# Optimization experiments

Hardware: AMD Instinct MI355X
Metric: run time of the kernel (lower is better)

Reference implementation:

```python
import jax, jax.numpy as jnp
import numpy as np

DIM = 2048
DIM_INNER = 4096
D_STATE = 64
D_CONV = 4
HEADDIM = 128
NHEADS = DIM_INNER // HEADDIM  # 32
CHUNK = 256
BATCH = 1
SEQ = 2048
CONV_DIM = DIM_INNER + 2 * D_STATE           # 4224
D_IN_PROJ = 2 * DIM_INNER + 2 * D_STATE + NHEADS  # 8352


def setup_inputs() -> dict:
    key = jax.random.key(0)
    ks = jax.random.split(key, 8)
    x = jax.random.normal(ks[0], (BATCH, SEQ, DIM), jnp.float32)
    in_proj_w = jax.random.normal(ks[1], (D_IN_PROJ, DIM), jnp.float32) * 0.02
    conv_w = jax.random.normal(ks[2], (CONV_DIM, D_CONV), jnp.float32) * 0.2
    conv_b = jnp.zeros((CONV_DIM,), jnp.float32)
    dt_bias = jax.random.normal(ks[3], (NHEADS,), jnp.float32) * 0.1
    A_log = jnp.log(jax.random.uniform(ks[4], (NHEADS,), jnp.float32, 1.0, 16.0))
    D = jnp.ones((NHEADS,), jnp.float32)
    norm_w = jnp.ones((DIM_INNER,), jnp.float32)
    out_proj_w = jax.random.normal(ks[5], (DIM, DIM_INNER), jnp.float32) * 0.02
    return dict(x=x, in_proj_w=in_proj_w, conv_w=conv_w, conv_b=conv_b,
                dt_bias=dt_bias, A_log=A_log, D=D, norm_w=norm_w,
                out_proj_w=out_proj_w)


def _segsum(a):
    # a: [..., T]; out[..., i, j] = sum_{k=j+1..i} a[..., k] for i>=j else -inf
    T = a.shape[-1]
    cs = jnp.cumsum(a, axis=-1)
    seg = cs[..., :, None] - cs[..., None, :]
    mask = jnp.tril(jnp.ones((T, T), bool))
    return jnp.where(mask, seg, -jnp.inf)


def _ssd(x, A, Bm, Cm, chunk):
    # x: [b,l,h,p], A: [b,l,h], Bm/Cm: [b,l,n] (ngroups=1, group dim squeezed)
    b, l, h, p = x.shape
    n = Bm.shape[-1]
    c = l // chunk
    x = x.reshape(b, c, chunk, h, p)
    A = A.reshape(b, c, chunk, h).transpose(0, 3, 1, 2)  # [b,h,c,l]
    Bm = Bm.reshape(b, c, chunk, n)
    Cm = Cm.reshape(b, c, chunk, n)
    A_cumsum = jnp.cumsum(A, axis=-1)                    # [b,h,c,l]
    Lmat = jnp.exp(_segsum(A))                           # [b,h,c,l,l]
    # intra-chunk (diagonal) contribution
    Y_diag = jnp.einsum('bcln,bcsn,bhcls,bcshp->bclhp', Cm, Bm, Lmat, x)
    # per-chunk states
    decay_states = jnp.exp(A_cumsum[..., -1:] - A_cumsum)
    states = jnp.einsum('bcln,bhcl,bclhp->bchpn', Bm, decay_states, x)
    states = jnp.concatenate([jnp.zeros_like(states[:, :1]), states], axis=1)
    # inter-chunk recurrence
    A_last = jnp.pad(A_cumsum[..., -1], ((0, 0), (0, 0), (1, 0)))  # [b,h,c+1]
    decay_chunk = jnp.exp(_segsum(A_last))
    new_states = jnp.einsum('bhzc,bchpn->bzhpn', decay_chunk, states)
    states, final_state = new_states[:, :-1], new_states[:, -1]
    # state -> output (off-diagonal) contribution
    state_decay_out = jnp.exp(A_cumsum)
    Y_off = jnp.einsum('bcln,bchpn,bhcl->bclhp', Cm, states, state_decay_out)
    return (Y_diag + Y_off).reshape(b, l, h, p), final_state


def reference(x, in_proj_w, conv_w, conv_b, dt_bias, A_log, D, norm_w, out_proj_w):
    B, L, _ = x.shape
    zxbcdt = x @ in_proj_w.T                              # [B,L,8352]
    z = zxbcdt[..., :DIM_INNER]
    xBC = zxbcdt[..., DIM_INNER:DIM_INNER + CONV_DIM]
    dt = jax.nn.softplus(zxbcdt[..., -NHEADS:] + dt_bias)  # [B,L,H]
    # causal depthwise conv1d over time (pad d_conv-1 on the left)
    xc = xBC.transpose(0, 2, 1)                           # [B,conv_dim,L]
    xc = jax.lax.conv_general_dilated(
        xc, conv_w[:, None, :], (1,), [(D_CONV - 1, 0)],
        dimension_numbers=('NCH', 'OIH', 'NCH'), feature_group_count=CONV_DIM)
    xc = xc + conv_b[None, :, None]
    xBC = jax.nn.silu(xc).transpose(0, 2, 1)              # [B,L,conv_dim]
    xs = xBC[..., :DIM_INNER].reshape(B, L, NHEADS, HEADDIM)
    Bmat = xBC[..., DIM_INNER:DIM_INNER + D_STATE]
    Cmat = xBC[..., DIM_INNER + D_STATE:]
    A = -jnp.exp(A_log)                                   # [H]
    y, final_state = _ssd(xs * dt[..., None], A * dt, Bmat, Cmat, CHUNK)
    y = y + xs * D[:, None]
    y = y.reshape(B, L, DIM_INNER)
    # gated RMSNorm: x * silu(z), then rms_norm with weight
    g = y * jax.nn.silu(z)
    g = g * jax.lax.rsqrt(jnp.mean(g * g, axis=-1, keepdims=True) + 1e-5) * norm_w
    return g @ out_proj_w.T
```

## Files before the change

### kernel.cpp

```cpp
#include <hip/hip_runtime.h>

typedef short v8s __attribute__((ext_vector_type(8)));
typedef float v4f __attribute__((ext_vector_type(4)));

#define L_SEQ  2048
#define DPROJ  8352
#define CONVD  4224
#define DIN    4096
#define NH     32
#define HD     128
#define NSTATE 64
#define NCHUNK 8
#define CKLEN  256

#define GLOAD_LDS16(gp, lp) \
  __builtin_amdgcn_global_load_lds((const __attribute__((address_space(1))) void*)(gp), \
                                   (__attribute__((address_space(3))) void*)(lp), 16, 0, 0)

__device__ __forceinline__ unsigned short to_bf16(float f) {
  unsigned u = __float_as_uint(f);
  return (unsigned short)((u + 0x7fffu + ((u >> 16) & 1u)) >> 16);
}

__global__ void cvt_bf16_kernel(const float* __restrict__ in,
                                unsigned short* __restrict__ out, int n) {
  int i = (blockIdx.x * 256 + threadIdx.x) * 8;
  if (i + 8 <= n) {
    float4 a = *(const float4*)(in + i);
    float4 b = *(const float4*)(in + i + 4);
    v8s r;
    r[0] = (short)to_bf16(a.x); r[1] = (short)to_bf16(a.y);
    r[2] = (short)to_bf16(a.z); r[3] = (short)to_bf16(a.w);
    r[4] = (short)to_bf16(b.x); r[5] = (short)to_bf16(b.y);
    r[6] = (short)to_bf16(b.z); r[7] = (short)to_bf16(b.w);
    *(v8s*)(out + i) = r;
  }
}


#define BAR    __builtin_amdgcn_s_barrier()
#define SCHEDB __builtin_amdgcn_sched_barrier(0)
#define LGKM0  asm volatile("s_waitcnt lgkmcnt(0)" ::: "memory")
#define VMCNT4 asm volatile("s_waitcnt vmcnt(4)" ::: "memory")

#define RDA(bu, mh) do { \
  _Pragma("unroll") \
  for (int i = 0; i < 4; ++i) \
    _Pragma("unroll") \
    for (int s = 0; s < 2; ++s) { \
      int row_ = (mh) * 128 + wm * 64 + i * 16 + lrow; \
      int off_ = row_ * 128 + s * 64 + lquad * 16; \
      off_ ^= ((off_ >> 9) & 1) << 5; \
      a8[i][s] = *(const v8s*)((const char*)smem + (bu) * 32768 + off_); \
    } \
} while (0)

#define RDB(bu, nh) do { \
  _Pragma("unroll") \
  for (int j = 0; j < 2; ++j) \
    _Pragma("unroll") \
    for (int s = 0; s < 2; ++s) { \
      int row_ = (nh) * 128 + wn * 32 + j * 16 + lrow; \
      int off_ = row_ * 128 + s * 64 + lquad * 16; \
      off_ ^= ((off_ >> 9) & 1) << 5; \
      b8[nh][j][s] = *(const v8s*)((const char*)smem + 65536 + (bu) * 32768 + off_); \
    } \
} while (0)

#define MM(mh, nh) do { \
  __builtin_amdgcn_s_setprio(1); \
  _Pragma("unroll") \
  for (int i = 0; i < 4; ++i) \
    _Pragma("unroll") \
    for (int j = 0; j < 2; ++j) \
      _Pragma("unroll") \
      for (int s = 0; s < 2; ++s) \
        acc[(mh)*4+i][(nh)*2+j] = __builtin_amdgcn_mfma_f32_16x16x32_bf16( \
            a8[i][s], b8[(nh)][j][s], acc[(mh)*4+i][(nh)*2+j], 0, 0, 0); \
  __builtin_amdgcn_s_setprio(0); \
} while (0)

#define KSTEP(BU, BN_, T1, T2) do { \
  RDA(BU, 0); RDB(BU, 0); \
  stA(BN_, 1, T1); \
  BAR; SCHEDB; LGKM0; SCHEDB; \
  MM(0, 0); \
  BAR; SCHEDB; \
  RDB(BU, 1); \
  stB(BN_, 1, T1); \
  BAR; SCHEDB; LGKM0; SCHEDB; \
  MM(0, 1); \
  BAR; SCHEDB; \
  RDA(BU, 1); \
  stA(BU, 0, T2); \
  BAR; SCHEDB; LGKM0; SCHEDB; \
  MM(1, 0); \
  BAR; SCHEDB; \
  stB(BU, 0, T2); \
  BAR; SCHEDB; \
  MM(1, 1); \
  VMCNT4; SCHEDB; \
  BAR; SCHEDB; \
} while (0)

__global__ __launch_bounds__(512, 2) void gemm_nt_256(
    const unsigned short* __restrict__ A, const unsigned short* __restrict__ B,
    float* __restrict__ C, int M, int N, int K)
{
  __shared__ unsigned short smem[65536];
  const int m0 = blockIdx.x * 256;
  const int n0 = blockIdx.y * 256;
  const int tid = threadIdx.x;
  const int wave = tid >> 6, lane = tid & 63;
  const int wm = wave >> 2, wn = wave & 3;
  const int lrow = lane & 15, lquad = lane >> 4;
  const int NT = K >> 6;

  v4f acc[8][4] = {};
  v8s a8[4][2];
  v8s b8[2][2][2];

  auto stA = [&](int bu, int h, int kt) {
#pragma unroll
    for (int g = 0; g < 2; ++g) {
      int lin = h * 16384 + g * 8192 + tid * 16;
      int sw = lin ^ (((lin >> 9) & 1) << 5);
      int row = sw >> 7;
      const unsigned short* src = A + (size_t)(m0 + row) * K + kt * 64 + ((sw & 127) >> 1);
      GLOAD_LDS16(src, smem + bu * 16384 + h * 8192 + g * 4096 + wave * 512);
    }
  };
  auto stB = [&](int bu, int h, int kt) {
#pragma unroll
    for (int g = 0; g < 2; ++g) {
      int lin = h * 16384 + g * 8192 + tid * 16;
      int sw = lin ^ (((lin >> 9) & 1) << 5);
      int brow = n0 + (sw >> 7);
      if (brow >= N) brow = N - 1;
      const unsigned short* src = B + (size_t)brow * K + kt * 64 + ((sw & 127) >> 1);
      GLOAD_LDS16(src, smem + 32768 + bu * 16384 + h * 8192 + g * 4096 + wave * 512);
    }
  };

  stA(0, 0, 0); stA(0, 1, 0); stB(0, 0, 0); stB(0, 1, 0);
  stA(1, 0, 1); stB(1, 0, 1);
  VMCNT4; SCHEDB; BAR; SCHEDB;

#pragma unroll 1
  for (int tt = 0; tt < NT; tt += 2) {
    {
      int t1 = tt + 1;
      int t2 = (tt + 2 < NT) ? tt + 2 : NT - 1;
      KSTEP(0, 1, t1, t2);
    }
    {
      int t1 = (tt + 2 < NT) ? tt + 2 : NT - 1;
      int t2 = (tt + 3 < NT) ? tt + 3 : NT - 1;
      KSTEP(1, 0, t1, t2);
    }
  }

#pragma unroll
  for (int mh = 0; mh < 2; ++mh)
#pragma unroll
    for (int i = 0; i < 4; ++i) {
      int grow = m0 + mh * 128 + wm * 64 + i * 16 + lquad * 4;
#pragma unroll
      for (int nh = 0; nh < 2; ++nh)
#pragma unroll
        for (int j = 0; j < 2; ++j) {
          int gcol = n0 + nh * 128 + wn * 32 + j * 16 + lrow;
          if (gcol < N) {
#pragma unroll
            for (int r = 0; r < 4; ++r)
              C[(size_t)(grow + r) * N + gcol] = acc[mh * 4 + i][nh * 2 + j][r];
          }
        }
    }
}

__global__ __launch_bounds__(256) void gemm_nt_bf16_64(
    const unsigned short* __restrict__ A, const unsigned short* __restrict__ B,
    float* __restrict__ C, int M, int N, int K)
{
  __shared__ unsigned short As[64 * 32];
  __shared__ unsigned short Bs[128 * 32];
  const int m0 = blockIdx.x * 64;
  const int n0 = blockIdx.y * 128;
  const int tid = threadIdx.x;
  const int wave = tid >> 6, lane = tid & 63;
  const int wm = (wave & 1) * 32, wn = (wave >> 1) * 64;
  const int lrow = lane & 15, lquad = lane >> 4;

  v4f acc[2][4] = {};

  for (int k0 = 0; k0 < K; k0 += 32) {
    __syncthreads();
    {
      int e = wave * 64 + lane;
      int row = e >> 2;
      int kq = (e & 3) * 8;
      const unsigned short* ap = A + (size_t)(m0 + row) * K + k0 + kq;
      GLOAD_LDS16(ap, As + wave * 512);
    }
#pragma unroll
    for (int r = 0; r < 2; ++r) {
      int e = wave * 128 + r * 64 + lane;
      int row = e >> 2;
      int kq = (e & 3) * 8;
      const unsigned short* bp = B + (size_t)(n0 + row) * K + k0 + kq;
      GLOAD_LDS16(bp, Bs + wave * 1024 + r * 512);
    }
    __syncthreads();
    v8s af[2], bfr[4];
#pragma unroll
    for (int i = 0; i < 2; ++i)
      af[i] = *(const v8s*)&As[(wm + i * 16 + lrow) * 32 + lquad * 8];
#pragma unroll
    for (int j = 0; j < 4; ++j)
      bfr[j] = *(const v8s*)&Bs[(wn + j * 16 + lrow) * 32 + lquad * 8];
#pragma unroll
    for (int i = 0; i < 2; ++i)
#pragma unroll
      for (int j = 0; j < 4; ++j)
        acc[i][j] = __builtin_amdgcn_mfma_f32_16x16x32_bf16(af[i], bfr[j], acc[i][j], 0, 0, 0);
  }

#pragma unroll
  for (int i = 0; i < 2; ++i) {
    int grow = m0 + wm + i * 16 + lquad * 4;
#pragma unroll
    for (int j = 0; j < 4; ++j) {
      int gcol = n0 + wn + j * 16 + lrow;
#pragma unroll
      for (int r = 0; r < 4; ++r)
        C[(size_t)(grow + r) * N + gcol] = acc[i][j][r];
    }
  }
}

__global__ __launch_bounds__(256) void conv_silu_kernel(
    const float* __restrict__ zx, const float* __restrict__ cw,
    const float* __restrict__ cb, float* __restrict__ out)
{
  const int l0 = blockIdx.x * 32, c0 = blockIdx.y * 128;
  const int tid = threadIdx.x;
  __shared__ float zs[35][128];
  __shared__ float cwl[4][128];
  __shared__ float cbl[128];
  for (int e = tid; e < 35 * 128; e += 256) {
    int k = e >> 7, cc = e & 127;
    int l = l0 + k - 3;
    zs[k][cc] = (l >= 0) ? zx[(size_t)l * DPROJ + DIN + c0 + cc] : 0.f;
  }
  for (int e = tid; e < 512; e += 256)
    cwl[e & 3][e >> 2] = cw[c0 * 4 + e];
  if (tid < 128) cbl[tid] = cb[c0 + tid];
  __syncthreads();
#pragma unroll
  for (int i = 0; i < 16; ++i) {
    int idx = i * 256 + tid;
    int ll = idx >> 7, cc = idx & 127;
    float acc = cbl[cc];
#pragma unroll
    for (int j = 0; j < 4; ++j)
      acc += zs[ll + j][cc] * cwl[j][cc];
    out[(size_t)(l0 + ll) * CONVD + c0 + cc] = acc / (1.f + __expf(-acc));
  }
}

__global__ void dt_kernel(const float* __restrict__ zx,
                          const float* __restrict__ dtb,
                          float* __restrict__ dt)
{
  int e = blockIdx.x * 256 + threadIdx.x;
  int l = e >> 5, h = e & 31;
  float v = zx[(size_t)l * DPROJ + (DPROJ - NH) + h] + dtb[h];
  dt[e] = (v > 20.f) ? v : log1pf(__expf(v));
}

__global__ void acum_kernel(const float* __restrict__ dt,
                            const float* __restrict__ alog,
                            float* __restrict__ acum)
{
  int h = blockIdx.x & 31, c = blockIdx.x >> 5;
  int t = threadIdx.x;
  int l = c * CKLEN + t;
  float A = -__expf(alog[h]);
  __shared__ float s[256];
  s[t] = A * dt[l * NH + h];
  __syncthreads();
  for (int off = 1; off < 256; off <<= 1) {
    float add = (t >= off) ? s[t - off] : 0.f;
    __syncthreads();
    s[t] += add;
    __syncthreads();
  }
  acum[h * L_SEQ + l] = s[t];
}

__global__ __launch_bounds__(256) void prep_kernel(
    const float* __restrict__ xbc, const float* __restrict__ dt,
    const float* __restrict__ acum, unsigned short* __restrict__ Xd,
    unsigned short* __restrict__ Btw, unsigned short* __restrict__ Cbf)
{
  const int h = blockIdx.x & 31, c = blockIdx.x >> 5;
  const int tid = threadIdx.x;
  __shared__ float Ac[256], Dt[256], Wd[256];
  __shared__ float Xs[32][129];
  __shared__ float Bs2[32][65];
  int l = c * CKLEN + tid;
  float a = acum[h * L_SEQ + l];
  Ac[tid] = a;
  Dt[tid] = dt[l * NH + h];
  __syncthreads();
  float alast = Ac[255];
  Wd[tid] = __expf(fminf(alast - a, 0.f));
  __syncthreads();
  unsigned short* XdB = Xd + (size_t)(c * NH + h) * (HD * CKLEN);
  unsigned short* BtB = Btw + (size_t)(c * NH + h) * (NSTATE * CKLEN);
  for (int t0 = 0; t0 < CKLEN; t0 += 32) {
    for (int e = tid; e < 32 * 128; e += 256) {
      int tt = e >> 7, pp = e & 127;
      Xs[tt][pp] = xbc[(size_t)(c * CKLEN + t0 + tt) * CONVD + h * HD + pp];
    }
    for (int e = tid; e < 32 * 64; e += 256) {
      int tt = e >> 6, nn = e & 63;
      Bs2[tt][nn] = xbc[(size_t)(c * CKLEN + t0 + tt) * CONVD + DIN + nn];
    }
    __syncthreads();
    {
      int p = tid >> 1, th = (tid & 1) * 16;
      v8s r0, r1;
#pragma unroll
      for (int k = 0; k < 8; ++k) {
        r0[k] = (short)to_bf16(Xs[th + k][p] * Dt[t0 + th + k]);
        r1[k] = (short)to_bf16(Xs[th + 8 + k][p] * Dt[t0 + th + 8 + k]);
      }
      *(v8s*)&XdB[p * CKLEN + t0 + th] = r0;
      *(v8s*)&XdB[p * CKLEN + t0 + th + 8] = r1;
    }
    {
      int n = tid >> 2, tq = (tid & 3) * 8;
      v8s r;
#pragma unroll
      for (int k = 0; k < 8; ++k)
        r[k] = (short)to_bf16(Bs2[tq + k][n] * Wd[t0 + tq + k]);
      *(v8s*)&BtB[n * CKLEN + t0 + tq] = r;
    }
    __syncthreads();
  }
  if (h == 0) {
    for (int e = tid; e < CKLEN * NSTATE; e += 256) {
      int ll = e >> 6, nn = e & 63;
      Cbf[(size_t)c * (CKLEN * NSTATE) + e] =
          to_bf16(xbc[(size_t)(c * CKLEN + ll) * CONVD + DIN + NSTATE + nn]);
    }
  }
}

__global__ __launch_bounds__(256) void g_kernel(const float* __restrict__ xbc,
                                                float* __restrict__ G)
{
  int c = blockIdx.z;
  int l0 = blockIdx.y * 64, s0 = blockIdx.x * 64;
  __shared__ float Cs[64][65];
  __shared__ float Bs[64][65];
  int tid = threadIdx.x;
  for (int e = tid; e < 64 * 64; e += 256) {
    int r = e >> 6, k = e & 63;
    Cs[r][k] = xbc[(size_t)(c * CKLEN + l0 + r) * CONVD + DIN + NSTATE + k];
    Bs[r][k] = xbc[(size_t)(c * CKLEN + s0 + r) * CONVD + DIN + k];
  }
  __syncthreads();
  int tx = tid & 15, ty = tid >> 4;
  float acc[4][4] = {};
  for (int k = 0; k < 64; ++k) {
    float a[4], b[4];
#pragma unroll
    for (int i = 0; i < 4; ++i) a[i] = Cs[ty * 4 + i][k];
#pragma unroll
    for (int j = 0; j < 4; ++j) b[j] = Bs[tx * 4 + j][k];
#pragma unroll
    for (int i = 0; i < 4; ++i)
#pragma unroll
      for (int j = 0; j < 4; ++j) acc[i][j] += a[i] * b[j];
  }
  for (int i = 0; i < 4; ++i)
    for (int j = 0; j < 4; ++j)
      G[((size_t)c * CKLEN + l0 + ty * 4 + i) * CKLEN + s0 + tx * 4 + j] = acc[i][j];
}

__global__ __launch_bounds__(256) void gexp_kernel_v2(
    const float* __restrict__ G, const float* __restrict__ acum,
    unsigned short* __restrict__ Gexp)
{
  const int b = blockIdx.x;
  const int si = b & 7, li = (b >> 3) & 3, c = b >> 5;
  const int l0 = li * 64, s0 = si * 32;
  const int tid = threadIdx.x;
  const int r = tid >> 2, sc = (tid & 3) * 8;

  if (s0 >= l0 + 64) {
    v8s z = {};
    for (int h = 0; h < NH; ++h)
      *(v8s*)&Gexp[(size_t)(c * NH + h) * 65536 + (size_t)(l0 + r) * 256 + s0 + sc] = z;
    return;
  }

  __shared__ float Gs[64 * 32];
  __shared__ float Acl[32][64];
  __shared__ float Acs[32][32];
  for (int e = tid; e < 2048; e += 256) {
    int rr = e >> 5, cc = e & 31;
    Gs[e] = G[(size_t)c * 65536 + (size_t)(l0 + rr) * 256 + s0 + cc];
  }
  for (int e = tid; e < 2048; e += 256) {
    int hh = e >> 6, rr = e & 63;
    Acl[hh][rr] = acum[hh * L_SEQ + c * CKLEN + l0 + rr];
  }
  for (int e = tid; e < 1024; e += 256) {
    int hh = e >> 5, ss = e & 31;
    Acs[hh][ss] = acum[hh * L_SEQ + c * CKLEN + s0 + ss];
  }
  __syncthreads();

  float g8[8];
#pragma unroll
  for (int k = 0; k < 8; ++k) g8[k] = Gs[r * 32 + sc + k];

  for (int h = 0; h < NH; ++h) {
    float al = Acl[h][r];
    v8s o;
#pragma unroll
    for (int k = 0; k < 8; ++k) {
      int s = s0 + sc + k;
      float m = 0.f;
      if (s <= l0 + r) m = g8[k] * __expf(fminf(al - Acs[h][sc + k], 0.f));
      o[k] = (short)to_bf16(m);
    }
    *(v8s*)&Gexp[(size_t)(c * NH + h) * 65536 + (size_t)(l0 + r) * 256 + s0 + sc] = o;
  }
}

__global__ __launch_bounds__(256) void states_kernel_v2(
    const unsigned short* __restrict__ Xd, const unsigned short* __restrict__ Btw,
    float* __restrict__ st)
{
  const int h = blockIdx.x & 31, c = blockIdx.x >> 5;
  const int tid = threadIdx.x;
  const int wave = tid >> 6, lane = tid & 63;
  const int wm = (wave & 1) * 64, wn = (wave >> 1) * 32;
  const int lrow = lane & 15, lquad = lane >> 4;

  __shared__ unsigned short As[128 * 32];
  __shared__ unsigned short Bs[64 * 32];
  const unsigned short* Ab = Xd + (size_t)(c * NH + h) * (HD * CKLEN);
  const unsigned short* Bb = Btw + (size_t)(c * NH + h) * (NSTATE * CKLEN);

  v4f acc[4][2] = {};

  for (int k0 = 0; k0 < CKLEN; k0 += 32) {
    __syncthreads();
#pragma unroll
    for (int r = 0; r < 2; ++r) {
      int e = wave * 128 + r * 64 + lane;
      int row = e >> 2, kq = (e & 3) * 8;
      GLOAD_LDS16(Ab + (size_t)row * CKLEN + k0 + kq, As + wave * 1024 + r * 512);
    }
    {
      int e = wave * 64 + lane;
      int row = e >> 2, kq = (e & 3) * 8;
      GLOAD_LDS16(Bb + (size_t)row * CKLEN + k0 + kq, Bs + wave * 512);
    }
    __syncthreads();
    v8s af[4], bfr[2];
#pragma unroll
    for (int i = 0; i < 4; ++i)
      af[i] = *(const v8s*)&As[(wm + i * 16 + lrow) * 32 + lquad * 8];
#pragma unroll
    for (int j = 0; j < 2; ++j)
      bfr[j] = *(const v8s*)&Bs[(wn + j * 16 + lrow) * 32 + lquad * 8];
#pragma unroll
    for (int i = 0; i < 4; ++i)
#pragma unroll
      for (int j = 0; j < 2; ++j)
        acc[i][j] = __builtin_amdgcn_mfma_f32_16x16x32_bf16(af[i], bfr[j], acc[i][j], 0, 0, 0);
  }

  float* outp = st + (size_t)(c * NH + h) * (HD * NSTATE);
#pragma unroll
  for (int i = 0; i < 4; ++i) {
    int p0 = wm + i * 16 + lquad * 4;
#pragma unroll
    for (int j = 0; j < 2; ++j) {
      int n = wn + j * 16 + lrow;
#pragma unroll
      for (int r = 0; r < 4; ++r)
        outp[(size_t)(p0 + r) * NSTATE + n] = acc[i][j][r];
    }
  }
}

__global__ void scan_kernel(const float* __restrict__ acum,
                            const float* __restrict__ st,
                            unsigned short* __restrict__ spbf)
{
  int e = blockIdx.x * 256 + threadIdx.x;
  int h = e >> 13;
  float running = 0.f;
#pragma unroll
  for (int c = 0; c < NCHUNK; ++c) {
    spbf[(size_t)c * 262144 + e] = to_bf16(running);
    float dec = __expf(fminf(acum[h * L_SEQ + c * CKLEN + 255], 0.f));
    running = running * dec + st[(size_t)c * 262144 + e];
  }
}

__global__ __launch_bounds__(256) void y_kernel_v2(
    const unsigned short* __restrict__ Gexp, const unsigned short* __restrict__ Xd,
    const unsigned short* __restrict__ Cbf, const unsigned short* __restrict__ spbf,
    const float* __restrict__ xbc, const float* __restrict__ acum,
    const float* __restrict__ Dp, float* __restrict__ Y)
{
  const int b = blockIdx.x, h = blockIdx.y, c = blockIdx.z;
  const int tid = threadIdx.x;
  const int wave = tid >> 6, lane = tid & 63;
  const int wm = wave * 32;
  const int lrow = lane & 15, lquad = lane >> 4;

  __shared__ unsigned short As[128 * 32];
  __shared__ unsigned short Bs[128 * 32];

  v4f acc[2][8] = {};

  const unsigned short* Ca = Cbf + (size_t)c * (CKLEN * NSTATE) + (size_t)b * 128 * NSTATE;
  const unsigned short* Sb = spbf + (size_t)(c * NH + h) * (HD * NSTATE);
  for (int n0 = 0; n0 < NSTATE; n0 += 32) {
    __syncthreads();
#pragma unroll
    for (int r = 0; r < 2; ++r) {
      int e = wave * 128 + r * 64 + lane;
      int row = e >> 2, kq = (e & 3) * 8;
      GLOAD_LDS16(Ca + (size_t)row * NSTATE + n0 + kq, As + wave * 1024 + r * 512);
      GLOAD_LDS16(Sb + (size_t)row * NSTATE + n0 + kq, Bs + wave * 1024 + r * 512);
    }
    __syncthreads();
    v8s af[2], bfr[8];
#pragma unroll
    for (int i = 0; i < 2; ++i)
      af[i] = *(const v8s*)&As[(wm + i * 16 + lrow) * 32 + lquad * 8];
#pragma unroll
    for (int j = 0; j < 8; ++j)
      bfr[j] = *(const v8s*)&Bs[(j * 16 + lrow) * 32 + lquad * 8];
#pragma unroll
    for (int i = 0; i < 2; ++i)
#pragma unroll
      for (int j = 0; j < 8; ++j)
        acc[i][j] = __builtin_amdgcn_mfma_f32_16x16x32_bf16(af[i], bfr[j], acc[i][j], 0, 0, 0);
  }

#pragma unroll
  for (int i = 0; i < 2; ++i) {
#pragma unroll
    for (int r = 0; r < 4; ++r) {
      int Lg = c * CKLEN + b * 128 + wm + i * 16 + lquad * 4 + r;
      float eA = __expf(fminf(acum[h * L_SEQ + Lg], 0.f));
#pragma unroll
      for (int j = 0; j < 8; ++j) acc[i][j][r] *= eA;
    }
  }

  const unsigned short* Ga = Gexp + (size_t)(c * NH + h) * (CKLEN * CKLEN)
                           + (size_t)b * 128 * CKLEN;
  const unsigned short* Xb = Xd + (size_t)(c * NH + h) * (HD * CKLEN);

  const int smax = (b + 1) * 128;
  for (int s0 = 0; s0 < smax; s0 += 32) {
    __syncthreads();
#pragma unroll
    for (int r = 0; r < 2; ++r) {
      int e = wave * 128 + r * 64 + lane;
      int row = e >> 2, kq = (e & 3) * 8;
      GLOAD_LDS16(Ga + (size_t)row * CKLEN + s0 + kq, As + wave * 1024 + r * 512);
      GLOAD_LDS16(Xb + (size_t)row * CKLEN + s0 + kq, Bs + wave * 1024 + r * 512);
    }
    __syncthreads();
    if (s0 <= b * 128 + wm + 31) {
      v8s af[2], bfr[8];
#pragma unroll
      for (int i = 0; i < 2; ++i)
        af[i] = *(const v8s*)&As[(wm + i * 16 + lrow) * 32 + lquad * 8];
#pragma unroll
      for (int j = 0; j < 8; ++j)
        bfr[j] = *(const v8s*)&Bs[(j * 16 + lrow) * 32 + lquad * 8];
#pragma unroll
      for (int i = 0; i < 2; ++i)
#pragma unroll
        for (int j = 0; j < 8; ++j)
          acc[i][j] = __builtin_amdgcn_mfma_f32_16x16x32_bf16(af[i], bfr[j], acc[i][j], 0, 0, 0);
    }
  }

  const float Dh = Dp[h];
#pragma unroll
  for (int i = 0; i < 2; ++i) {
#pragma unroll
    for (int j = 0; j < 8; ++j) {
      int p = j * 16 + lrow;
#pragma unroll
      for (int r = 0; r < 4; ++r) {
        int Lg = c * CKLEN + b * 128 + wm + i * 16 + lquad * 4 + r;
        float xs = xbc[(size_t)Lg * CONVD + h * HD + p];
        Y[(size_t)Lg * DIN + h * HD + p] = acc[i][j][r] + Dh * xs;
      }
    }
  }
}

__global__ __launch_bounds__(256) void norm_gate_kernel(const float* __restrict__ Y,
                                                        const float* __restrict__ zx,
                                                        const float* __restrict__ nw,
                                                        unsigned short* __restrict__ gbf)
{
  int l = blockIdx.x;
  int t = threadIdx.x;
  float g[16];
  float ss = 0.f;
#pragma unroll
  for (int i = 0; i < 16; ++i) {
    int idx = i * 256 + t;
    float z = zx[(size_t)l * DPROJ + idx];
    float y = Y[(size_t)l * DIN + idx];
    float gv = y * (z / (1.f + __expf(-z)));
    g[i] = gv;
    ss += gv * gv;
  }
#pragma unroll
  for (int off = 32; off > 0; off >>= 1) ss += __shfl_down(ss, off);
  __shared__ float red[4];
  if ((t & 63) == 0) red[t >> 6] = ss;
  __syncthreads();
  float total = red[0] + red[1] + red[2] + red[3];
  float scale = rsqrtf(total / (float)DIN + 1e-5f);
#pragma unroll
  for (int i = 0; i < 16; ++i) {
    int idx = i * 256 + t;
    gbf[(size_t)l * DIN + idx] = to_bf16(g[i] * scale * nw[idx]);
  }
}

extern "C" void kernel_launch(void* const* d_in, const int* in_sizes, int n_in,
                              void* d_out, int out_size, void* d_ws, size_t ws_size,
                              hipStream_t stream) {
  const float* x    = (const float*)d_in[0];
  const float* w1   = (const float*)d_in[1];
  const float* cw   = (const float*)d_in[2];
  const float* cb   = (const float*)d_in[3];
  const float* dtb  = (const float*)d_in[4];
  const float* alog = (const float*)d_in[5];
  const float* Dp   = (const float*)d_in[6];
  const float* nw   = (const float*)d_in[7];
  const float* w2   = (const float*)d_in[8];
  float* out = (float*)d_out;
  float* ws  = (float*)d_ws;

  unsigned short* xbf  = (unsigned short*)(ws + 0);
  unsigned short* w1bf = (unsigned short*)(ws + 2097152);
  unsigned short* Gexp = (unsigned short*)(ws + 0);
  unsigned short* Btw  = (unsigned short*)(ws + 8388608);
  unsigned short* w2bf = (unsigned short*)(ws + 10649600);
  float* zx   = ws + 14843904;
  float* xbc  = ws + 31948800;
  float* dt   = ws + 40599552;
  float* acum = ws + 40665088;
  float* G    = ws + 40730624;
  float* st   = ws + 41254912;
  float* Y    = ws + 43352064;
  unsigned short* gbf  = (unsigned short*)(ws + 51740672);
  unsigned short* Xd   = (unsigned short*)(ws + 53837824);
  unsigned short* Cbf  = (unsigned short*)(ws + 58032128);
  unsigned short* spbf = (unsigned short*)(ws + 58097664);

  cvt_bf16_kernel<<<4194304 / 2048, 256, 0, stream>>>(x, xbf, 4194304);
  cvt_bf16_kernel<<<17104896 / 2048, 256, 0, stream>>>(w1, w1bf, 17104896);
  cvt_bf16_kernel<<<8388608 / 2048, 256, 0, stream>>>(w2, w2bf, 8388608);

  gemm_nt_256<<<dim3(8, 33), 512, 0, stream>>>(xbf, w1bf, zx, 2048, 8352, 2048);

  conv_silu_kernel<<<dim3(64, 33), 256, 0, stream>>>(zx, cw, cb, xbc);
  dt_kernel<<<(L_SEQ * NH) / 256, 256, 0, stream>>>(zx, dtb, dt);
  acum_kernel<<<NCHUNK * NH, 256, 0, stream>>>(dt, alog, acum);

  prep_kernel<<<NCHUNK * NH, 256, 0, stream>>>(xbc, dt, acum, Xd, Btw, Cbf);
  g_kernel<<<dim3(4, 4, NCHUNK), 256, 0, stream>>>(xbc, G);
  gexp_kernel_v2<<<256, 256, 0, stream>>>(G, acum, Gexp);

  states_kernel_v2<<<NCHUNK * NH, 256, 0, stream>>>(Xd, Btw, st);
  scan_kernel<<<262144 / 256, 256, 0, stream>>>(acum, st, spbf);
  y_kernel_v2<<<dim3(2, NH, NCHUNK), 256, 0, stream>>>(Gexp, Xd, Cbf, spbf, xbc, acum, Dp, Y);

  norm_gate_kernel<<<L_SEQ, 256, 0, stream>>>(Y, zx, nw, gbf);

  gemm_nt_bf16_64<<<dim3(32, 16), 256, 0, stream>>>(gbf, w2bf, out, 2048, 2048, 4096);
}
```

Before: 498.4 us.

## Split-K out_proj with 256-tile GEMM, split in_proj tail, wider LDS swizzle

The out_proj GEMM moves from the small 64x128 kernel to the 256x256 pipelined kernel with split-K by 4 over blockIdx.z, followed by a reduction kernel that sums the four partial outputs. The in_proj GEMM now runs on a 32-column-tile grid with no ragged tile, and the last 160 columns go to a 64x128 tail kernel. The LDS XOR swizzle changes from one bit to three bits to cut bank conflicts. The split-K path adds about 64MB of partial-sum traffic plus an extra launch, in exchange for better MFMA utilisation.

```diff
diff --git a/kernel.cpp b/kernel.cpp
--- a/kernel.cpp
+++ b/kernel.cpp
@@ -50,7 +50,7 @@
     for (int s = 0; s < 2; ++s) { \
       int row_ = (mh) * 128 + wm * 64 + i * 16 + lrow; \
       int off_ = row_ * 128 + s * 64 + lquad * 16; \
-      off_ ^= ((off_ >> 9) & 1) << 5; \
+      off_ ^= ((off_ >> 7) & 7) << 4; \
       a8[i][s] = *(const v8s*)((const char*)smem + (bu) * 32768 + off_); \
     } \
 } while (0)
@@ -62,7 +62,7 @@
     for (int s = 0; s < 2; ++s) { \
       int row_ = (nh) * 128 + wn * 32 + j * 16 + lrow; \
       int off_ = row_ * 128 + s * 64 + lquad * 16; \
-      off_ ^= ((off_ >> 9) & 1) << 5; \
+      off_ ^= ((off_ >> 7) & 7) << 4; \
       b8[nh][j][s] = *(const v8s*)((const char*)smem + 65536 + (bu) * 32768 + off_); \
     } \
 } while (0)
@@ -105,11 +105,14 @@
 
 __global__ __launch_bounds__(512, 2) void gemm_nt_256(
     const unsigned short* __restrict__ A, const unsigned short* __restrict__ B,
-    float* __restrict__ C, int M, int N, int K)
+    float* __restrict__ C, int lda, int ldb, int ldc, int ncols, int K)
 {
   __shared__ unsigned short smem[65536];
   const int m0 = blockIdx.x * 256;
   const int n0 = blockIdx.y * 256;
+  A += (size_t)blockIdx.z * K;
+  B += (size_t)blockIdx.z * K;
+  C += (size_t)blockIdx.z * 2048 * (size_t)ldc;
   const int tid = threadIdx.x;
   const int wave = tid >> 6, lane = tid & 63;
   const int wm = wave >> 2, wn = wave & 3;
@@ -124,9 +127,9 @@
 #pragma unroll
     for (int g = 0; g < 2; ++g) {
       int lin = h * 16384 + g * 8192 + tid * 16;
-      int sw = lin ^ (((lin >> 9) & 1) << 5);
+      int sw = lin ^ (((lin >> 7) & 7) << 4);
       int row = sw >> 7;
-      const unsigned short* src = A + (size_t)(m0 + row) * K + kt * 64 + ((sw & 127) >> 1);
+      const unsigned short* src = A + (size_t)(m0 + row) * lda + kt * 64 + ((sw & 127) >> 1);
       GLOAD_LDS16(src, smem + bu * 16384 + h * 8192 + g * 4096 + wave * 512);
     }
   };
@@ -134,10 +137,10 @@
 #pragma unroll
     for (int g = 0; g < 2; ++g) {
       int lin = h * 16384 + g * 8192 + tid * 16;
-      int sw = lin ^ (((lin >> 9) & 1) << 5);
+      int sw = lin ^ (((lin >> 7) & 7) << 4);
       int brow = n0 + (sw >> 7);
-      if (brow >= N) brow = N - 1;
-      const unsigned short* src = B + (size_t)brow * K + kt * 64 + ((sw & 127) >> 1);
+      if (brow >= ncols) brow = ncols - 1;
+      const unsigned short* src = B + (size_t)brow * ldb + kt * 64 + ((sw & 127) >> 1);
       GLOAD_LDS16(src, smem + 32768 + bu * 16384 + h * 8192 + g * 4096 + wave * 512);
     }
   };
@@ -170,18 +173,37 @@
 #pragma unroll
         for (int j = 0; j < 2; ++j) {
           int gcol = n0 + nh * 128 + wn * 32 + j * 16 + lrow;
-          if (gcol < N) {
+          if (gcol < ncols) {
 #pragma unroll
             for (int r = 0; r < 4; ++r)
-              C[(size_t)(grow + r) * N + gcol] = acc[mh * 4 + i][nh * 2 + j][r];
+              C[(size_t)(grow + r) * ldc + gcol] = acc[mh * 4 + i][nh * 2 + j][r];
           }
         }
     }
 }
 
-__global__ __launch_bounds__(256) void gemm_nt_bf16_64(
+__global__ __launch_bounds__(256) void reduce_k4_kernel(
+    const float* __restrict__ p, float* __restrict__ out, int n)
+{
+  const int S = 4194304;
+  int i = (blockIdx.x * 256 + threadIdx.x) * 4;
+  if (i + 4 <= n) {
+    float4 a = *(const float4*)(p + i);
+    float4 b = *(const float4*)(p + S + i);
+    float4 c = *(const float4*)(p + 2 * S + i);
+    float4 d = *(const float4*)(p + 3 * S + i);
+    float4 o;
+    o.x = a.x + b.x + c.x + d.x;
+    o.y = a.y + b.y + c.y + d.y;
+    o.z = a.z + b.z + c.z + d.z;
+    o.w = a.w + b.w + c.w + d.w;
+    *(float4*)(out + i) = o;
+  }
+}
+
+__global__ __launch_bounds__(256) void gemm_nt_64tail(
     const unsigned short* __restrict__ A, const unsigned short* __restrict__ B,
-    float* __restrict__ C, int M, int N, int K)
+    float* __restrict__ C, int Ncols, int ldc, int K)
 {
   __shared__ unsigned short As[64 * 32];
   __shared__ unsigned short Bs[128 * 32];
@@ -208,7 +230,8 @@
       int e = wave * 128 + r * 64 + lane;
       int row = e >> 2;
       int kq = (e & 3) * 8;
-      const unsigned short* bp = B + (size_t)(n0 + row) * K + k0 + kq;
+      int br = n0 + row; if (br >= Ncols) br = Ncols - 1;
+      const unsigned short* bp = B + (size_t)br * K + k0 + kq;
       GLOAD_LDS16(bp, Bs + wave * 1024 + r * 512);
     }
     __syncthreads();
@@ -232,9 +255,11 @@
 #pragma unroll
     for (int j = 0; j < 4; ++j) {
       int gcol = n0 + wn + j * 16 + lrow;
-#pragma unroll
-      for (int r = 0; r < 4; ++r)
-        C[(size_t)(grow + r) * N + gcol] = acc[i][j][r];
+      if (gcol < Ncols) {
+#pragma unroll
+        for (int r = 0; r < 4; ++r)
+          C[(size_t)(grow + r) * ldc + gcol] = acc[i][j][r];
+      }
     }
   }
 }
@@ -671,6 +696,7 @@
   unsigned short* Btw  = (unsigned short*)(ws + 8388608);
   unsigned short* w2bf = (unsigned short*)(ws + 10649600);
   float* zx   = ws + 14843904;
+  float* part = ws + 14843904;
   float* xbc  = ws + 31948800;
   float* dt   = ws + 40599552;
   float* acum = ws + 40665088;
@@ -686,7 +712,10 @@
   cvt_bf16_kernel<<<17104896 / 2048, 256, 0, stream>>>(w1, w1bf, 17104896);
   cvt_bf16_kernel<<<8388608 / 2048, 256, 0, stream>>>(w2, w2bf, 8388608);
 
-  gemm_nt_256<<<dim3(8, 33), 512, 0, stream>>>(xbf, w1bf, zx, 2048, 8352, 2048);
+  gemm_nt_256<<<dim3(8, 32, 1), 512, 0, stream>>>(
+      xbf, w1bf, zx, 2048, 2048, 8352, 8352, 2048);
+  gemm_nt_64tail<<<dim3(32, 2), 256, 0, stream>>>(
+      xbf, w1bf + (size_t)8192 * 2048, zx + 8192, 160, 8352, 2048);
 
   conv_silu_kernel<<<dim3(64, 33), 256, 0, stream>>>(zx, cw, cb, xbc);
   dt_kernel<<<(L_SEQ * NH) / 256, 256, 0, stream>>>(zx, dtb, dt);
@@ -702,5 +731,7 @@
 
   norm_gate_kernel<<<L_SEQ, 256, 0, stream>>>(Y, zx, nw, gbf);
 
-  gemm_nt_bf16_64<<<dim3(32, 16), 256, 0, stream>>>(gbf, w2bf, out, 2048, 2048, 4096);
-}
+  gemm_nt_256<<<dim3(8, 8, 4), 512, 0, stream>>>(
+      gbf, w2bf, part, 4096, 4096, 2048, 2048, 1024);
+  reduce_k4_kernel<<<4194304 / 1024, 256, 0, stream>>>(part, out, 4194304);
+}
```

Result: faster. 452.1 us (-9.3%).
